# Kernel tuning notes

Measured on AMD Instinct MI355X. Metric: run time of the kernel, lower is better.

Reference implementation:

```python
import jax, jax.numpy as jnp
import numpy as np

B, N, K, D, DEG = 16, 4096, 64, 128, 16  # graphs, nodes/graph, clusters, feat dim, avg degree
E = B * N * DEG


def setup_inputs() -> dict:
    key = jax.random.key(0)
    k0, k1, k2, k3, k4, k5 = jax.random.split(key, 6)
    x = jax.random.normal(k0, (B * N, D), dtype=jnp.float32)
    W = jax.random.normal(k1, (D, K), dtype=jnp.float32) / np.sqrt(D)
    b = jnp.zeros((K,), dtype=jnp.float32)
    # edges strictly within each graph, then offset by graph start
    offs = (jnp.arange(B) * N)[:, None]                      # [B,1]
    src = jax.random.randint(k2, (B, N * DEG), 0, N) + offs  # [B, N*DEG]
    dst = jax.random.randint(k3, (B, N * DEG), 0, N) + offs
    edge_index = jnp.stack([src.reshape(-1), dst.reshape(-1)], axis=0)  # [2,E]
    edge_weight = jax.random.uniform(k4, (E,), dtype=jnp.float32)
    batch_ptr = jnp.arange(B + 1, dtype=jnp.int64) * N
    # pre-sampled uniforms for gumbel noise (constant across fwd/bwd like torch)
    gumbel_u = jax.random.uniform(k5, (B * N, K), dtype=jnp.float32, minval=1e-6, maxval=1.0)
    return {"x": x, "W": W, "b": b, "edge_weight": edge_weight, "gumbel_u": gumbel_u,
            "edge_index": edge_index, "batch_ptr": batch_ptr}


def reference(x, W, b, edge_weight, gumbel_u, edge_index, batch_ptr):
    Ntot, Dd = x.shape
    Kk = W.shape[1]
    Bn = batch_ptr.shape[0] - 1
    Nn = Ntot // Bn  # equal-sized graphs

    # pooling net + hard gumbel-softmax (tau=1, straight-through)
    logits = x @ W + b                                   # [Ntot,K]
    g = -jnp.log(-jnp.log(gumbel_u))
    y_soft = jax.nn.softmax(logits + g, axis=-1)
    y_hard = jax.nn.one_hot(jnp.argmax(y_soft, axis=-1), Kk, dtype=y_soft.dtype)
    s = y_hard + y_soft - jax.lax.stop_gradient(y_soft)  # forward == one-hot

    sb = s.reshape(Bn, Nn, Kk)
    xb = x.reshape(Bn, Nn, Dd)
    out = jnp.einsum('bnk,bnd->bkd', sb, xb).reshape(Bn * Kk, Dd)

    src, dst = edge_index[0], edge_index[1]
    # A @ S via scatter over src, then S^T (A S) per graph
    AS = jax.ops.segment_sum(edge_weight[:, None] * s[dst], src, num_segments=Ntot)  # [Ntot,K]
    out_adj = jnp.einsum('bnk,bnl->bkl', sb, AS.reshape(Bn, Nn, Kk))                 # [B,K,K]

    # link loss: ||A - S S^T||_F per graph = sqrt(||A||^2 - 2<A,SS^T> + ||S^T S||^2)
    ge = src // Nn                                        # graph id per edge
    a_sq = jax.ops.segment_sum(edge_weight ** 2, ge, num_segments=Bn)
    cross = jax.ops.segment_sum(edge_weight * jnp.einsum('ek,ek->e', s[src], s[dst]), ge, num_segments=Bn)
    StS = jnp.einsum('bnk,bnl->bkl', sb, sb)
    sst_sq = jnp.sum(StS ** 2, axis=(1, 2))
    e_per = jax.ops.segment_sum(jnp.ones_like(edge_weight), ge, num_segments=Bn)
    link = jnp.sqrt(jnp.maximum(a_sq - 2.0 * cross + sst_sq, 0.0)) / e_per  # normalize=True
    link_loss = jnp.mean(link)

    ent = (-s * jnp.log(s + 1e-15)).sum(-1).reshape(Bn, Nn).mean(-1)
    entropy_loss = jnp.mean(ent)

    batch = jnp.repeat(jnp.arange(Bn), Kk)
    batch_ptr_out = jnp.arange(Bn + 1) * Kk
    return out, out_adj, link_loss, entropy_loss, batch, batch_ptr_out
```

## Files before the change

kernel.cpp:

```cpp
#include <hip/hip_runtime.h>

#define NGRAPH 16
#define NPG    4096
#define KCL    64
#define DF     128
#define NTOT   65536
#define NEDGE  1048576


#define WS_CLUS   0
#define WS_CNT    65536
#define WS_START  69632
#define WS_CROSS  73728
#define WS_ASQ    74752
#define WS_ORDER  75776
#define WS_ADJP   206848

__global__ __launch_bounds__(256) void assign_kernel(
    const float* __restrict__ x, const float* __restrict__ W,
    const float* __restrict__ bias, const float* __restrict__ gum,
    unsigned char* __restrict__ clus)
{
    __shared__ __align__(16) float xs[64 * 132];
    __shared__ float cand_v[4][64];
    __shared__ int   cand_k[4][64];

    const int tid = threadIdx.x, wave = tid >> 6, lane = tid & 63;
    const int n0 = blockIdx.x * 64;

    {
        const float4* xg = (const float4*)(x + (size_t)n0 * DF);
        #pragma unroll
        for (int i = 0; i < 8; ++i) {
            int j4 = tid + i * 256; int j = j4 << 2;
            float4 v = xg[j4];
            *(float4*)&xs[(j >> 7) * 132 + (j & 127)] = v;
        }
    }
    __syncthreads();

    const int k0 = __builtin_amdgcn_readfirstlane(wave << 4);
    float acc[16];
    #pragma unroll
    for (int kk = 0; kk < 16; ++kk) acc[kk] = bias[k0 + kk];

    #pragma unroll 4
    for (int dc = 0; dc < 32; ++dc) {
        float4 xv = *(const float4*)&xs[lane * 132 + (dc << 2)];
        const float* wp = W + (dc << 8) + k0;
        #pragma unroll
        for (int kk = 0; kk < 16; ++kk) {
            float a = acc[kk];
            a = fmaf(xv.x, wp[kk],        a);
            a = fmaf(xv.y, wp[64  + kk],  a);
            a = fmaf(xv.z, wp[128 + kk],  a);
            a = fmaf(xv.w, wp[192 + kk],  a);
            acc[kk] = a;
        }
    }

    const float* gp = gum + ((size_t)(n0 + lane) << 6) + k0;
    float best = -3.4e38f; int bestk = k0;
    #pragma unroll
    for (int q = 0; q < 4; ++q) {
        float4 u = *(const float4*)(gp + (q << 2));
        float uv[4] = {u.x, u.y, u.z, u.w};
        #pragma unroll
        for (int r = 0; r < 4; ++r) {
            float g = -__logf(-__logf(uv[r]));
            float v = acc[(q << 2) + r] + g;
            if (v > best) { best = v; bestk = k0 + (q << 2) + r; }
        }
    }
    cand_v[wave][lane] = best;
    cand_k[wave][lane] = bestk;
    __syncthreads();

    if (tid < 64) {
        float bv = cand_v[0][tid]; int bk = cand_k[0][tid];
        #pragma unroll
        for (int w2 = 1; w2 < 4; ++w2) {
            float v = cand_v[w2][tid];
            if (v > bv) { bv = v; bk = cand_k[w2][tid]; }
        }
        clus[n0 + tid] = (unsigned char)bk;
    }
}

__global__ __launch_bounds__(1024) void sortedge_kernel(
    const unsigned char* __restrict__ clus,
    const int* __restrict__ ei, const float* __restrict__ ew,
    int* __restrict__ counts, int* __restrict__ starts,
    unsigned short* __restrict__ order,
    float* __restrict__ adjp, float* __restrict__ crossp,
    float* __restrict__ asqp)
{
    __shared__ int   hist[KCL];
    __shared__ int   offs[KCL];
    __shared__ float adj[KCL * KCL];
    __shared__ unsigned char cl[NPG];
    __shared__ float redc[16], redq[16];

    const int tid = threadIdx.x;

    if (blockIdx.x < 16) {
        const int bg = blockIdx.x;
        if (tid < KCL) hist[tid] = 0;
        __syncthreads();
        unsigned char c[4];
        #pragma unroll
        for (int i = 0; i < 4; ++i) {
            c[i] = clus[(bg << 12) + tid + (i << 10)];
            atomicAdd(&hist[c[i]], 1);
        }
        __syncthreads();
        if (tid < KCL) {
            int v = hist[tid], inc = v;
            #pragma unroll
            for (int off = 1; off < 64; off <<= 1) {
                int t = __shfl_up(inc, off);
                if (tid >= off) inc += t;
            }
            int excl = inc - v;
            offs[tid] = excl;
            counts[(bg << 6) + tid] = v;
            starts[(bg << 6) + tid] = excl;
        }
        __syncthreads();
        #pragma unroll
        for (int i = 0; i < 4; ++i) {
            int p = atomicAdd(&offs[c[i]], 1);
            order[(bg << 12) + p] = (unsigned short)(tid + (i << 10));
        }
    } else {
        const int eb = blockIdx.x - 16;
        const int bg = eb >> 4;
        ((float4*)adj)[tid] = make_float4(0.f, 0.f, 0.f, 0.f);
        ((int*)cl)[tid] = ((const int*)(clus + (size_t)bg * NPG))[tid];
        __syncthreads();

        const int e0 = eb << 12;
        float csum = 0.f, qsum = 0.f;
        #pragma unroll
        for (int it = 0; it < 4; ++it) {
            const int e = e0 + (it << 10) + tid;
            const int s = ei[e]         & (NPG - 1);
            const int d = ei[NEDGE + e] & (NPG - 1);
            const float w = ew[e];
            const int ks = cl[s], kd = cl[d];
            atomicAdd(&adj[(ks << 6) + kd], w);
            csum += (ks == kd) ? w : 0.f;
            qsum += w * w;
        }
        #pragma unroll
        for (int off = 32; off > 0; off >>= 1) {
            csum += __shfl_down(csum, off);
            qsum += __shfl_down(qsum, off);
        }
        const int lane = tid & 63, wv = tid >> 6;
        if (lane == 0) { redc[wv] = csum; redq[wv] = qsum; }
        __syncthreads();
        if (tid == 0) {
            float cs = 0.f, qs = 0.f;
            #pragma unroll
            for (int i = 0; i < 16; ++i) { cs += redc[i]; qs += redq[i]; }
            crossp[eb] = cs;
            asqp[eb]   = qs;
        }
        ((float4*)(adjp + ((size_t)eb << 12)))[tid] = ((const float4*)adj)[tid];
    }
}

__global__ __launch_bounds__(256) void poolreduce_kernel(
    const float* __restrict__ x, const unsigned short* __restrict__ order,
    const int* __restrict__ counts, const int* __restrict__ starts,
    const float* __restrict__ adjp, const float* __restrict__ crossp,
    const float* __restrict__ asqp, float* __restrict__ out)
{
    __shared__ unsigned short ord[NPG];
    __shared__ float4 part[8][32];
    __shared__ float links[16];

    const int tid = threadIdx.x;
    const int blk = blockIdx.x;

    if (blk < 1024) {
        const int bg = blk >> 6, k = blk & 63;
        const int cnt = counts[blk], start = starts[blk];
        for (int i = tid; i < cnt; i += 256)
            ord[i] = order[(bg << 12) + start + i];
        __syncthreads();
        const int grp = tid >> 5, l32 = tid & 31;
        float4 acc = {0.f, 0.f, 0.f, 0.f};
        for (int i = grp; i < cnt; i += 8) {
            const float4* row = (const float4*)(x + (((size_t)(bg << 12) + ord[i]) << 7));
            float4 v = row[l32];
            acc.x += v.x; acc.y += v.y; acc.z += v.z; acc.w += v.w;
        }
        part[grp][l32] = acc;
        __syncthreads();
        if (grp == 0) {
            float4 s = part[0][l32];
            #pragma unroll
            for (int g = 1; g < 8; ++g) {
                float4 p = part[g][l32];
                s.x += p.x; s.y += p.y; s.z += p.z; s.w += p.w;
            }
            ((float4*)(out + ((size_t)(bg << 13) + (k << 7))))[l32] = s;
        }
    } else if (blk < 1280) {
        const int cell = ((blk - 1024) << 8) + tid;
        const int bg = cell >> 12, j = cell & 4095;
        float s = 0.f;
        #pragma unroll
        for (int sl = 0; sl < 16; ++sl)
            s += adjp[(size_t)(((bg << 4) + sl) << 12) + j];
        out[131072 + cell] = s;
    } else {
        if (tid < 16) {
            const int bg = tid;
            float s2 = 0.f;
            #pragma unroll 8
            for (int k = 0; k < 64; ++k) {
                float c = (float)counts[(bg << 6) + k];
                s2 = fmaf(c, c, s2);
            }
            float cs = 0.f, as = 0.f;
            #pragma unroll
            for (int sl = 0; sl < 16; ++sl) {
                cs += crossp[(bg << 4) + sl];
                as += asqp[(bg << 4) + sl];
            }
            links[bg] = sqrtf(fmaxf(as - 2.f * cs + s2, 0.f)) * (1.f / 65536.f);
        }
        __syncthreads();
        if (tid == 0) {
            float m = 0.f;
            #pragma unroll
            for (int i = 0; i < 16; ++i) m += links[i];
            out[196608] = m * (1.f / 16.f);
            out[196609] = 0.f;
        }
        #pragma unroll
        for (int r = 0; r < 4; ++r) {
            int i = tid + (r << 8);
            out[196610 + i] = (float)(i >> 6);
        }
        if (tid < 17) out[197634 + tid] = (float)(tid << 6);
    }
}

extern "C" void kernel_launch(void* const* d_in, const int* in_sizes, int n_in,
                              void* d_out, int out_size, void* d_ws, size_t ws_size,
                              hipStream_t stream) {
    const float* x    = (const float*)d_in[0];
    const float* W    = (const float*)d_in[1];
    const float* bias = (const float*)d_in[2];
    const float* ew   = (const float*)d_in[3];
    const float* gum  = (const float*)d_in[4];
    const int*   ei   = (const int*)  d_in[5];

    float* out = (float*)d_out;
    char*  wsb = (char*)d_ws;

    unsigned char*  clus   = (unsigned char*) (wsb + WS_CLUS);
    int*            counts = (int*)           (wsb + WS_CNT);
    int*            starts = (int*)           (wsb + WS_START);
    float*          crossp = (float*)         (wsb + WS_CROSS);
    float*          asqp   = (float*)         (wsb + WS_ASQ);
    unsigned short* order  = (unsigned short*)(wsb + WS_ORDER);
    float*          adjp   = (float*)         (wsb + WS_ADJP);

    assign_kernel<<<NTOT / 64, 256, 0, stream>>>(x, W, bias, gum, clus);

    sortedge_kernel<<<16 + 256, 1024, 0, stream>>>(
        clus, ei, ew, counts, starts, order, adjp, crossp, asqp);

    poolreduce_kernel<<<1024 + 256 + 1, 256, 0, stream>>>(
        x, order, counts, starts, adjp, crossp, asqp, out);
}
```

Measured before the change: 132.0 us.

## Fuse three kernels into one cooperative kernel with grid-wide syncs

Merges the assignment, sort/edge-histogram and pooling/reduction kernels into one cooperative kernel of 256 blocks of 1024 threads, separated by grid.sync barriers. Work is remapped so each block handles four 64-node tiles, one edge slice, and four cluster rows, with shared memory reused through a union. This targets the launch gaps between kernels but adds grid-barrier cost, limits the grid to one block per CU, and lowers per-phase occupancy. The large shared footprint (about 140KB for the assign phase) may exceed the per-block LDS limit.

```diff
diff --git a/kernel.cpp b/kernel.cpp
--- a/kernel.cpp
+++ b/kernel.cpp
@@ -1,4 +1,7 @@
 #include <hip/hip_runtime.h>
+#include <hip/hip_cooperative_groups.h>
+
+namespace cg = cooperative_groups;
 
 #define NGRAPH 16
 #define NPG    4096
@@ -16,127 +19,152 @@
 #define WS_ORDER  75776
 #define WS_ADJP   206848
 
-__global__ __launch_bounds__(256) void assign_kernel(
+
+struct P1 {
+    float xs[4][64 * 132];
+    float cv[4][4][64];
+    int   ck[4][4][64];
+};
+struct P2 {
+    int   hist[KCL];
+    int   offs[KCL];
+    float adj[KCL * KCL];
+    unsigned char cl[NPG];
+    float redc[16], redq[16];
+};
+struct P3 {
+    unsigned short ord[4][NPG];
+    float4 part[4][8][32];
+};
+union ShU { P1 p1; P2 p2; P3 p3; };
+
+__global__ __launch_bounds__(1024) void fused_kernel(
     const float* __restrict__ x, const float* __restrict__ W,
     const float* __restrict__ bias, const float* __restrict__ gum,
-    unsigned char* __restrict__ clus)
+    const float* __restrict__ ew, const int* __restrict__ ei,
+    float* __restrict__ out, char* __restrict__ wsb)
 {
-    __shared__ __align__(16) float xs[64 * 132];
-    __shared__ float cand_v[4][64];
-    __shared__ int   cand_k[4][64];
-
-    const int tid = threadIdx.x, wave = tid >> 6, lane = tid & 63;
-    const int n0 = blockIdx.x * 64;
+    __shared__ ShU sh;
+    cg::grid_group grid = cg::this_grid();
+
+    unsigned char*  clus   = (unsigned char*) (wsb + WS_CLUS);
+    int*            counts = (int*)           (wsb + WS_CNT);
+    int*            starts = (int*)           (wsb + WS_START);
+    float*          crossp = (float*)         (wsb + WS_CROSS);
+    float*          asqp   = (float*)         (wsb + WS_ASQ);
+    unsigned short* order  = (unsigned short*)(wsb + WS_ORDER);
+    float*          adjp   = (float*)         (wsb + WS_ADJP);
+
+    const int tid = threadIdx.x;
+    const int blk = blockIdx.x;
 
     {
-        const float4* xg = (const float4*)(x + (size_t)n0 * DF);
-        #pragma unroll
-        for (int i = 0; i < 8; ++i) {
-            int j4 = tid + i * 256; int j = j4 << 2;
-            float4 v = xg[j4];
-            *(float4*)&xs[(j >> 7) * 132 + (j & 127)] = v;
+        const int sub  = tid >> 8;
+        const int t    = tid & 255;
+        const int wave = (tid >> 6) & 3;
+        const int lane = tid & 63;
+        const int n0   = (blk << 8) + (sub << 6);
+        float* xs = sh.p1.xs[sub];
+
+        {
+            const float4* xg = (const float4*)(x + (size_t)n0 * DF);
+            #pragma unroll
+            for (int i = 0; i < 8; ++i) {
+                int j4 = t + (i << 8); int j = j4 << 2;
+                float4 v = xg[j4];
+                *(float4*)&xs[(j >> 7) * 132 + (j & 127)] = v;
+            }
+        }
+        __syncthreads();
+
+        const int k0 = __builtin_amdgcn_readfirstlane(wave << 4);
+        float acc[16];
+        #pragma unroll
+        for (int kk = 0; kk < 16; ++kk) acc[kk] = bias[k0 + kk];
+
+        #pragma unroll 4
+        for (int dc = 0; dc < 32; ++dc) {
+            float4 xv = *(const float4*)&xs[lane * 132 + (dc << 2)];
+            const float* wp = W + (dc << 8) + k0;
+            #pragma unroll
+            for (int kk = 0; kk < 16; ++kk) {
+                float a = acc[kk];
+                a = fmaf(xv.x, wp[kk],        a);
+                a = fmaf(xv.y, wp[64  + kk],  a);
+                a = fmaf(xv.z, wp[128 + kk],  a);
+                a = fmaf(xv.w, wp[192 + kk],  a);
+                acc[kk] = a;
+            }
+        }
+
+        const float* gp = gum + ((size_t)(n0 + lane) << 6) + k0;
+        float best = -3.4e38f; int bestk = k0;
+        #pragma unroll
+        for (int q = 0; q < 4; ++q) {
+            float4 u = *(const float4*)(gp + (q << 2));
+            float uv[4] = {u.x, u.y, u.z, u.w};
+            #pragma unroll
+            for (int r = 0; r < 4; ++r) {
+                float g = -__logf(-__logf(uv[r]));
+                float v = acc[(q << 2) + r] + g;
+                if (v > best) { best = v; bestk = k0 + (q << 2) + r; }
+            }
+        }
+        sh.p1.cv[sub][wave][lane] = best;
+        sh.p1.ck[sub][wave][lane] = bestk;
+        __syncthreads();
+
+        if (t < 64) {
+            float bv = sh.p1.cv[sub][0][t]; int bk = sh.p1.ck[sub][0][t];
+            #pragma unroll
+            for (int w2 = 1; w2 < 4; ++w2) {
+                float v = sh.p1.cv[sub][w2][t];
+                if (v > bv) { bv = v; bk = sh.p1.ck[sub][w2][t]; }
+            }
+            clus[n0 + t] = (unsigned char)bk;
         }
     }
     __syncthreads();
-
-    const int k0 = __builtin_amdgcn_readfirstlane(wave << 4);
-    float acc[16];
-    #pragma unroll
-    for (int kk = 0; kk < 16; ++kk) acc[kk] = bias[k0 + kk];
-
-    #pragma unroll 4
-    for (int dc = 0; dc < 32; ++dc) {
-        float4 xv = *(const float4*)&xs[lane * 132 + (dc << 2)];
-        const float* wp = W + (dc << 8) + k0;
-        #pragma unroll
-        for (int kk = 0; kk < 16; ++kk) {
-            float a = acc[kk];
-            a = fmaf(xv.x, wp[kk],        a);
-            a = fmaf(xv.y, wp[64  + kk],  a);
-            a = fmaf(xv.z, wp[128 + kk],  a);
-            a = fmaf(xv.w, wp[192 + kk],  a);
-            acc[kk] = a;
-        }
-    }
-
-    const float* gp = gum + ((size_t)(n0 + lane) << 6) + k0;
-    float best = -3.4e38f; int bestk = k0;
-    #pragma unroll
-    for (int q = 0; q < 4; ++q) {
-        float4 u = *(const float4*)(gp + (q << 2));
-        float uv[4] = {u.x, u.y, u.z, u.w};
-        #pragma unroll
-        for (int r = 0; r < 4; ++r) {
-            float g = -__logf(-__logf(uv[r]));
-            float v = acc[(q << 2) + r] + g;
-            if (v > best) { best = v; bestk = k0 + (q << 2) + r; }
-        }
-    }
-    cand_v[wave][lane] = best;
-    cand_k[wave][lane] = bestk;
-    __syncthreads();
-
-    if (tid < 64) {
-        float bv = cand_v[0][tid]; int bk = cand_k[0][tid];
-        #pragma unroll
-        for (int w2 = 1; w2 < 4; ++w2) {
-            float v = cand_v[w2][tid];
-            if (v > bv) { bv = v; bk = cand_k[w2][tid]; }
-        }
-        clus[n0 + tid] = (unsigned char)bk;
-    }
-}
-
-__global__ __launch_bounds__(1024) void sortedge_kernel(
-    const unsigned char* __restrict__ clus,
-    const int* __restrict__ ei, const float* __restrict__ ew,
-    int* __restrict__ counts, int* __restrict__ starts,
-    unsigned short* __restrict__ order,
-    float* __restrict__ adjp, float* __restrict__ crossp,
-    float* __restrict__ asqp)
-{
-    __shared__ int   hist[KCL];
-    __shared__ int   offs[KCL];
-    __shared__ float adj[KCL * KCL];
-    __shared__ unsigned char cl[NPG];
-    __shared__ float redc[16], redq[16];
-
-    const int tid = threadIdx.x;
-
-    if (blockIdx.x < 16) {
-        const int bg = blockIdx.x;
-        if (tid < KCL) hist[tid] = 0;
-        __syncthreads();
-        unsigned char c[4];
-        #pragma unroll
-        for (int i = 0; i < 4; ++i) {
-            c[i] = clus[(bg << 12) + tid + (i << 10)];
-            atomicAdd(&hist[c[i]], 1);
-        }
-        __syncthreads();
-        if (tid < KCL) {
-            int v = hist[tid], inc = v;
-            #pragma unroll
-            for (int off = 1; off < 64; off <<= 1) {
-                int t = __shfl_up(inc, off);
-                if (tid >= off) inc += t;
-            }
-            int excl = inc - v;
-            offs[tid] = excl;
-            counts[(bg << 6) + tid] = v;
-            starts[(bg << 6) + tid] = excl;
-        }
-        __syncthreads();
-        #pragma unroll
-        for (int i = 0; i < 4; ++i) {
-            int p = atomicAdd(&offs[c[i]], 1);
-            order[(bg << 12) + p] = (unsigned short)(tid + (i << 10));
-        }
-    } else {
-        const int eb = blockIdx.x - 16;
+    __threadfence();
+    grid.sync();
+
+    {
+        if (blk < 16) {
+            const int bg = blk;
+            if (tid < KCL) sh.p2.hist[tid] = 0;
+            __syncthreads();
+            unsigned char c[4];
+            #pragma unroll
+            for (int i = 0; i < 4; ++i) {
+                c[i] = clus[(bg << 12) + tid + (i << 10)];
+                atomicAdd(&sh.p2.hist[c[i]], 1);
+            }
+            __syncthreads();
+            if (tid < KCL) {
+                int v = sh.p2.hist[tid], inc = v;
+                #pragma unroll
+                for (int off = 1; off < 64; off <<= 1) {
+                    int tt = __shfl_up(inc, off);
+                    if (tid >= off) inc += tt;
+                }
+                int excl = inc - v;
+                sh.p2.offs[tid] = excl;
+                counts[(bg << 6) + tid] = v;
+                starts[(bg << 6) + tid] = excl;
+            }
+            __syncthreads();
+            #pragma unroll
+            for (int i = 0; i < 4; ++i) {
+                int p = atomicAdd(&sh.p2.offs[c[i]], 1);
+                order[(bg << 12) + p] = (unsigned short)(tid + (i << 10));
+            }
+            __syncthreads();
+        }
+
+        const int eb = blk;
         const int bg = eb >> 4;
-        ((float4*)adj)[tid] = make_float4(0.f, 0.f, 0.f, 0.f);
-        ((int*)cl)[tid] = ((const int*)(clus + (size_t)bg * NPG))[tid];
+        ((float4*)sh.p2.adj)[tid] = make_float4(0.f, 0.f, 0.f, 0.f);
+        ((int*)sh.p2.cl)[tid] = ((const int*)(clus + (size_t)bg * NPG))[tid];
         __syncthreads();
 
         const int e0 = eb << 12;
@@ -147,8 +175,8 @@
             const int s = ei[e]         & (NPG - 1);
             const int d = ei[NEDGE + e] & (NPG - 1);
             const float w = ew[e];
-            const int ks = cl[s], kd = cl[d];
-            atomicAdd(&adj[(ks << 6) + kd], w);
+            const int ks = sh.p2.cl[s], kd = sh.p2.cl[d];
+            atomicAdd(&sh.p2.adj[(ks << 6) + kd], w);
             csum += (ks == kd) ? w : 0.f;
             qsum += w * w;
         }
@@ -158,94 +186,87 @@
             qsum += __shfl_down(qsum, off);
         }
         const int lane = tid & 63, wv = tid >> 6;
-        if (lane == 0) { redc[wv] = csum; redq[wv] = qsum; }
+        if (lane == 0) { sh.p2.redc[wv] = csum; sh.p2.redq[wv] = qsum; }
         __syncthreads();
         if (tid == 0) {
             float cs = 0.f, qs = 0.f;
             #pragma unroll
-            for (int i = 0; i < 16; ++i) { cs += redc[i]; qs += redq[i]; }
+            for (int i = 0; i < 16; ++i) { cs += sh.p2.redc[i]; qs += sh.p2.redq[i]; }
             crossp[eb] = cs;
             asqp[eb]   = qs;
         }
-        ((float4*)(adjp + ((size_t)eb << 12)))[tid] = ((const float4*)adj)[tid];
-    }
-}
-
-__global__ __launch_bounds__(256) void poolreduce_kernel(
-    const float* __restrict__ x, const unsigned short* __restrict__ order,
-    const int* __restrict__ counts, const int* __restrict__ starts,
-    const float* __restrict__ adjp, const float* __restrict__ crossp,
-    const float* __restrict__ asqp, float* __restrict__ out)
-{
-    __shared__ unsigned short ord[NPG];
-    __shared__ float4 part[8][32];
-    __shared__ float links[16];
-
-    const int tid = threadIdx.x;
-    const int blk = blockIdx.x;
-
-    if (blk < 1024) {
-        const int bg = blk >> 6, k = blk & 63;
-        const int cnt = counts[blk], start = starts[blk];
-        for (int i = tid; i < cnt; i += 256)
-            ord[i] = order[(bg << 12) + start + i];
-        __syncthreads();
-        const int grp = tid >> 5, l32 = tid & 31;
-        float4 acc = {0.f, 0.f, 0.f, 0.f};
+        ((float4*)(adjp + ((size_t)eb << 12)))[tid] = ((const float4*)sh.p2.adj)[tid];
+    }
+    __syncthreads();
+    __threadfence();
+    grid.sync();
+
+    {
+        const int sub = tid >> 8, t = tid & 255;
+        const int u = (blk << 2) + sub;
+        const int bg = u >> 6, k = u & 63;
+        const int cnt = counts[u], start = starts[u];
+        unsigned short* ordS = sh.p3.ord[sub];
+        for (int i = t; i < cnt; i += 256)
+            ordS[i] = order[((size_t)bg << 12) + start + i];
+        __syncthreads();
+        const int grp = t >> 5, l32 = t & 31;
+        float4 acc = make_float4(0.f, 0.f, 0.f, 0.f);
         for (int i = grp; i < cnt; i += 8) {
-            const float4* row = (const float4*)(x + (((size_t)(bg << 12) + ord[i]) << 7));
+            const float4* row = (const float4*)(x + (((size_t)(bg << 12) + ordS[i]) << 7));
             float4 v = row[l32];
             acc.x += v.x; acc.y += v.y; acc.z += v.z; acc.w += v.w;
         }
-        part[grp][l32] = acc;
+        sh.p3.part[sub][grp][l32] = acc;
         __syncthreads();
         if (grp == 0) {
-            float4 s = part[0][l32];
+            float4 s = sh.p3.part[sub][0][l32];
             #pragma unroll
             for (int g = 1; g < 8; ++g) {
-                float4 p = part[g][l32];
+                float4 p = sh.p3.part[sub][g][l32];
                 s.x += p.x; s.y += p.y; s.z += p.z; s.w += p.w;
             }
-            ((float4*)(out + ((size_t)(bg << 13) + (k << 7))))[l32] = s;
-        }
-    } else if (blk < 1280) {
-        const int cell = ((blk - 1024) << 8) + tid;
+            ((float4*)(out + (((size_t)bg << 13) + (k << 7))))[l32] = s;
+        }
+    }
+
+    if (tid < 256) {
+        const int cell = (blk << 8) + tid;
         const int bg = cell >> 12, j = cell & 4095;
         float s = 0.f;
         #pragma unroll
         for (int sl = 0; sl < 16; ++sl)
-            s += adjp[(size_t)(((bg << 4) + sl) << 12) + j];
+            s += adjp[((size_t)((bg << 4) + sl) << 12) + j];
         out[131072 + cell] = s;
-    } else {
-        if (tid < 16) {
-            const int bg = tid;
-            float s2 = 0.f;
-            #pragma unroll 8
-            for (int k = 0; k < 64; ++k) {
-                float c = (float)counts[(bg << 6) + k];
-                s2 = fmaf(c, c, s2);
-            }
-            float cs = 0.f, as = 0.f;
-            #pragma unroll
-            for (int sl = 0; sl < 16; ++sl) {
-                cs += crossp[(bg << 4) + sl];
-                as += asqp[(bg << 4) + sl];
-            }
-            links[bg] = sqrtf(fmaxf(as - 2.f * cs + s2, 0.f)) * (1.f / 65536.f);
-        }
-        __syncthreads();
-        if (tid == 0) {
-            float m = 0.f;
-            #pragma unroll
-            for (int i = 0; i < 16; ++i) m += links[i];
-            out[196608] = m * (1.f / 16.f);
-            out[196609] = 0.f;
-        }
-        #pragma unroll
-        for (int r = 0; r < 4; ++r) {
-            int i = tid + (r << 8);
-            out[196610 + i] = (float)(i >> 6);
-        }
+    }
+
+    if (blk == 0) {
+        if (tid < 64) {
+            float link = 0.f;
+            if (tid < 16) {
+                const int bg = tid;
+                float s2 = 0.f;
+                #pragma unroll 8
+                for (int k2 = 0; k2 < 64; ++k2) {
+                    float c = (float)counts[(bg << 6) + k2];
+                    s2 = fmaf(c, c, s2);
+                }
+                float cs = 0.f, as = 0.f;
+                #pragma unroll
+                for (int sl = 0; sl < 16; ++sl) {
+                    cs += crossp[(bg << 4) + sl];
+                    as += asqp[(bg << 4) + sl];
+                }
+                link = sqrtf(fmaxf(as - 2.f * cs + s2, 0.f)) * (1.f / 65536.f);
+            }
+            #pragma unroll
+            for (int off = 8; off > 0; off >>= 1) link += __shfl_down(link, off);
+            if (tid == 0) {
+                out[196608] = link * (1.f / 16.f);
+                out[196609] = 0.f;
+            }
+        }
+        out[196610 + tid] = (float)(tid >> 6);
         if (tid < 17) out[197634 + tid] = (float)(tid << 6);
     }
 }
@@ -263,19 +284,8 @@
     float* out = (float*)d_out;
     char*  wsb = (char*)d_ws;
 
-    unsigned char*  clus   = (unsigned char*) (wsb + WS_CLUS);
-    int*            counts = (int*)           (wsb + WS_CNT);
-    int*            starts = (int*)           (wsb + WS_START);
-    float*          crossp = (float*)         (wsb + WS_CROSS);
-    float*          asqp   = (float*)         (wsb + WS_ASQ);
-    unsigned short* order  = (unsigned short*)(wsb + WS_ORDER);
-    float*          adjp   = (float*)         (wsb + WS_ADJP);
-
-    assign_kernel<<<NTOT / 64, 256, 0, stream>>>(x, W, bias, gum, clus);
-
-    sortedge_kernel<<<16 + 256, 1024, 0, stream>>>(
-        clus, ei, ew, counts, starts, order, adjp, crossp, asqp);
-
-    poolreduce_kernel<<<1024 + 256 + 1, 256, 0, stream>>>(
-        x, order, counts, starts, adjp, crossp, asqp, out);
+    void* args[8] = { (void*)&x, (void*)&W, (void*)&bias, (void*)&gum,
+                      (void*)&ew, (void*)&ei, (void*)&out, (void*)&wsb };
+    hipLaunchCooperativeKernel(fused_kernel, dim3(256), dim3(1024),
+                               args, 0, stream);
 }
```

Result: slower. 343.0 us (+159.9%).
